# Optimization experiments

Measured on AMD Instinct MI355X. Metric: run time of the kernel, lower is better.

## Reference

```python
import jax, jax.numpy as jnp
import numpy as np

B, T, D = 2, 2048, 1024
H = 16
HD = D // H
NE = 17  # n_edge_types + 1

def setup_inputs() -> dict:
    key = jax.random.key(0)
    ks = jax.random.split(key, 6)
    x = jax.random.normal(ks[0], (B, T, D), dtype=jnp.float32)
    graph_adj = jax.random.uniform(ks[1], (B, T, T), dtype=jnp.float32)
    edge_types = jax.random.randint(ks[2], (B, T, T), 0, NE, dtype=jnp.int32)
    Wqkv = jax.random.normal(ks[3], (D, 3 * D), dtype=jnp.float32) * (D ** -0.5)
    Wproj = jax.random.normal(ks[4], (D, D), dtype=jnp.float32) * (D ** -0.5)
    adj_bias = jnp.zeros((H,), dtype=jnp.float32)
    edge_table = jax.random.normal(ks[5], (NE, H), dtype=jnp.float32) * 0.02
    return {"x": x, "graph_adj": graph_adj, "edge_types": edge_types,
            "Wqkv": Wqkv, "Wproj": Wproj, "adj_bias": adj_bias,
            "edge_table": edge_table}

def reference(x, graph_adj, edge_types, Wqkv, Wproj, adj_bias, edge_table):
    Bc, Tc, C = x.shape
    qkv = (x @ Wqkv).reshape(Bc, Tc, 3, H, HD)
    q, k, v = qkv[:, :, 0], qkv[:, :, 1], qkv[:, :, 2]  # [B,T,H,HD]
    scale = 1.0 / jnp.sqrt(jnp.asarray(HD, dtype=x.dtype))
    # scores: [B,H,T,T]
    attn = jnp.einsum('bqhd,bkhd->bhqk', q, k) * scale
    # adjacency bias per head
    attn = attn + adj_bias[None, :, None, None] * graph_adj[:, None, :, :]
    # edge-type bias: lookup [B,T,T,H] -> [B,H,T,T]
    etype_b = edge_table[edge_types]  # [B,T,T,H]
    attn = attn + jnp.transpose(etype_b, (0, 3, 1, 2))
    # causal mask (upper triangle, diag=1)
    causal = jnp.triu(jnp.ones((Tc, Tc), dtype=bool), k=1)
    attn = jnp.where(causal[None, None, :, :], jnp.asarray(-jnp.inf, dtype=attn.dtype), attn)
    attn = jax.nn.softmax(attn, axis=-1)
    out = jnp.einsum('bhqk,bkhd->bqhd', attn, v).reshape(Bc, Tc, C)
    return out @ Wproj
```

## Files before the change

kernel.cpp:

```cpp
#include <hip/hip_runtime.h>
#include <stdint.h>

#define TT 2048
#define HH 16
#define LOG2E 1.44269504089f

typedef _Float16 f16;
typedef __attribute__((ext_vector_type(8))) _Float16 f16x8;
typedef __attribute__((ext_vector_type(4))) float f32x4;
typedef unsigned short ushort_t;

__device__ __forceinline__ void gl_lds16(const void* g, void* l){
  __builtin_amdgcn_global_load_lds(
      (__attribute__((address_space(1))) void*)(void*)g,
      (__attribute__((address_space(3))) void*)l, 16, 0, 0);
}

__device__ __forceinline__ void lds_barrier(){
  __asm__ volatile("s_waitcnt lgkmcnt(0)\n\ts_barrier" ::: "memory");
}

template<int CTRL>
__device__ __forceinline__ float dpp_mov(float x){
  int xi = __builtin_bit_cast(int, x);
  return __builtin_bit_cast(float,
      __builtin_amdgcn_update_dpp(xi, xi, CTRL, 0xF, 0xF, false));
}
__device__ __forceinline__ float row_red_max(float x){
  x = fmaxf(x, dpp_mov<0xB1>(x));
  x = fmaxf(x, dpp_mov<0x4E>(x));
  x = fmaxf(x, dpp_mov<0x124>(x));
  x = fmaxf(x, dpp_mov<0x128>(x));
  return x;
}
__device__ __forceinline__ float row_red_sum(float x){
  x += dpp_mov<0xB1>(x);
  x += dpp_mov<0x4E>(x);
  x += dpp_mov<0x124>(x);
  x += dpp_mov<0x128>(x);
  return x;
}

struct SchedT { unsigned short v[80]; };
static constexpr SchedT make_sched(){
  SchedT s{};
  int idx = 0;
  for (int size = 8; size >= 1; --size){
    for (int qt = 31; qt >= 8; --qt){
      int full = qt >> 3;
      int tail = (qt & 7) + 1;
      if (size == 8)
        for (int ci = 0; ci < full; ++ci)
          s.v[idx++] = (unsigned short)(qt | (ci << 8));
      if (tail == size)
        s.v[idx++] = (unsigned short)(qt | (full << 8));
    }
    s.v[idx++] = (unsigned short)(size - 1);
  }
  return s;
}
__constant__ SchedT SCHED = make_sched();

__device__ __forceinline__ int slot_base(int qt){
  return (qt < 16) ? 2 * (qt - 8)
       : (qt < 24) ? 16 + 3 * (qt - 16)
                   : 40 + 4 * (qt - 24);
}

__global__ __launch_bounds__(256) void cvt_f2h_kernel(const float4* __restrict__ in,
                                                      uint2* __restrict__ out, int n4){
  int i = blockIdx.x * 256 + threadIdx.x;
  if (i >= n4) return;
  float4 v = in[i];
  union { f16 h[4]; uint2 u; } o;
  o.h[0] = (f16)v.x; o.h[1] = (f16)v.y; o.h[2] = (f16)v.z; o.h[3] = (f16)v.w;
  out[i] = o.u;
}

__global__ __launch_bounds__(256) void pack_bias_kernel(const float* __restrict__ gadj,
                                                        const int* __restrict__ etype,
                                                        uint32_t* __restrict__ out){
  int bid = blockIdx.x;
  int b = bid / 528, ti = bid - b * 528;
  int qt = (int)((sqrtf(8.f * (float)ti + 1.f) - 1.f) * 0.5f);
  while ((qt + 1) * (qt + 2) / 2 <= ti) ++qt;
  while (qt * (qt + 1) / 2 > ti) --qt;
  int kt = ti - qt * (qt + 1) / 2;

  int t = threadIdx.x;
  int row = t >> 2, c0 = (t & 3) << 4;
  size_t src = ((size_t)b * TT + qt * 64 + row) * TT + kt * 64 + c0;
  uint32_t* dst = out + (size_t)bid * 4096;
  int wq = (row >> 4) * 64 + ((row & 15) >> 2) * 16;
  int jbase = (t & 3) * 4 + (row & 3);
  #pragma unroll
  for (int v4 = 0; v4 < 4; ++v4){
    float4 g = *(const float4*)(gadj + src + v4 * 4);
    int4   e = *(const int4*)(etype + src + v4 * 4);
    union { f16 h; ushort_t u; } c;
    c.h = (f16)g.x; dst[(wq + v4 * 4 + 0) * 16 + jbase] = (uint32_t)c.u | ((uint32_t)e.x << 16);
    c.h = (f16)g.y; dst[(wq + v4 * 4 + 1) * 16 + jbase] = (uint32_t)c.u | ((uint32_t)e.y << 16);
    c.h = (f16)g.z; dst[(wq + v4 * 4 + 2) * 16 + jbase] = (uint32_t)c.u | ((uint32_t)e.z << 16);
    c.h = (f16)g.w; dst[(wq + v4 * 4 + 3) * 16 + jbase] = (uint32_t)c.u | ((uint32_t)e.w << 16);
  }
}

__global__ __launch_bounds__(256) void transpose_cvt_kernel(const float* __restrict__ in,
                                                            f16* __restrict__ out, int R, int C){
  __shared__ float tile[64][65];
  int c0 = blockIdx.x * 64, r0 = blockIdx.y * 64;
  int t = threadIdx.x;
  int row = t >> 2, cs = (t & 3) << 4;
  const float4* src = (const float4*)(in + (size_t)(r0 + row) * C + c0 + cs);
  float4 a = src[0], b = src[1], c = src[2], d = src[3];
  float* tr = &tile[row][cs];
  tr[0]=a.x; tr[1]=a.y; tr[2]=a.z;  tr[3]=a.w;
  tr[4]=b.x; tr[5]=b.y; tr[6]=b.z;  tr[7]=b.w;
  tr[8]=c.x; tr[9]=c.y; tr[10]=c.z; tr[11]=c.w;
  tr[12]=d.x;tr[13]=d.y;tr[14]=d.z; tr[15]=d.w;
  __syncthreads();
  f16 tmp[16];
  #pragma unroll
  for (int j = 0; j < 16; ++j) tmp[j] = (f16)tile[cs + j][row];
  f16* dst = out + (size_t)(c0 + row) * R + r0 + cs;
  *(uint4*)dst = *(uint4*)&tmp[0];
  *(uint4*)(dst + 8) = *(uint4*)&tmp[8];
}

template<int BN>
__global__ __launch_bounds__(256) void gemm_f16_kernel(const f16* __restrict__ A,
                                                       const f16* __restrict__ Bt,
                                                       void* __restrict__ Cout,
                                                       int M, int N, int K, int out_f32){
  constexpr int WN = BN / 2;
  constexpr int NI = WN / 16;
  __shared__ __align__(16) f16 As[128 * 32];
  __shared__ __align__(16) f16 Bs[BN * 32];
  int t = threadIdx.x;
  int w = t >> 6, lane = t & 63;
  int wm = (w >> 1) * 64, wn = (w & 1) * WN;
  int lrow = lane & 15, quad = lane >> 4;
  int bm = blockIdx.y, bn = blockIdx.x;

  f32x4 acc[4][NI];
  for (int i = 0; i < 4; ++i)
    for (int j = 0; j < NI; ++j)
      for (int r = 0; r < 4; ++r) acc[i][j][r] = 0.f;

  const int nk = K >> 5;
  for (int kt = 0; kt < nk; ++kt){
    int k0 = kt << 5;
    __syncthreads();
    #pragma unroll
    for (int i = 0; i < 2; ++i){
      int c = (w << 7) + (i << 6) + lane;
      gl_lds16(A + (size_t)((bm << 7) + (c >> 2)) * K + k0 + ((c & 3) << 3),
               As + ((w << 7) + (i << 6)) * 8);
      if constexpr (BN == 128){
        gl_lds16(Bt + (size_t)((bn << 7) + (c >> 2)) * K + k0 + ((c & 3) << 3),
                 Bs + ((w << 7) + (i << 6)) * 8);
      }
    }
    if constexpr (BN == 64){
      int c = (w << 6) + lane;
      gl_lds16(Bt + (size_t)((bn << 6) + (c >> 2)) * K + k0 + ((c & 3) << 3),
               Bs + (w << 6) * 8);
    }
    __syncthreads();
    f16x8 af[4], bfr[NI];
    #pragma unroll
    for (int mi = 0; mi < 4; ++mi)
      af[mi] = *(const f16x8*)(As + (wm + mi * 16 + lrow) * 32 + quad * 8);
    #pragma unroll
    for (int ni = 0; ni < NI; ++ni)
      bfr[ni] = *(const f16x8*)(Bs + (wn + ni * 16 + lrow) * 32 + quad * 8);
    #pragma unroll
    for (int mi = 0; mi < 4; ++mi)
      #pragma unroll
      for (int ni = 0; ni < NI; ++ni)
        acc[mi][ni] = __builtin_amdgcn_mfma_f32_16x16x32_f16(af[mi], bfr[ni], acc[mi][ni], 0, 0, 0);
  }

  #pragma unroll
  for (int mi = 0; mi < 4; ++mi)
    #pragma unroll
    for (int ni = 0; ni < NI; ++ni)
      #pragma unroll
      for (int r = 0; r < 4; ++r){
        int row = (bm << 7) + wm + mi * 16 + quad * 4 + r;
        int col = bn * BN + wn + ni * 16 + lrow;
        float val = acc[mi][ni][r];
        if (out_f32) ((float*)Cout)[(size_t)row * N + col] = val;
        else         ((f16*)Cout)[(size_t)row * N + col] = (f16)val;
      }
}

__global__ __launch_bounds__(256, 4) void attn_kernel(const f16* __restrict__ qkv,
                                                      const uint32_t* __restrict__ pbias,
                                                      const float* __restrict__ adj_bias,
                                                      const float* __restrict__ edge_table,
                                                      f16* __restrict__ attn_out,
                                                      f16* __restrict__ Opart,
                                                      float* __restrict__ MLpart){
  __shared__ __align__(16) f16 Ks[64 * 72];
  __shared__ __align__(16) f16 Vt[64 * 72];
  __shared__ __align__(16) f16 Ps[4][16 * 72];
  __shared__ float edge_lds[32 * 17];

  int bx = blockIdx.x;
  int bh = bx & 31;
  int h = bh & 15, b = bh >> 4;
  int ej = SCHED.v[bx >> 5];
  int qt = ej & 31, ci = ej >> 8;
  int ksrt = ci << 3;
  int kend = min(qt, ksrt + 7);
  bool whole = (qt < 8);

  int t = threadIdx.x;
  int w = t >> 6, lane = t & 63;
  int lrow = lane & 15, quad = lane >> 4;

  for (int i = t; i < 544; i += 256)
    edge_lds[i] = edge_table[(i % 17) * HH + h] * LOG2E;
  float adjb = adj_bias[h] * LOG2E;
  int erep = (lane & 31) * 17;

  int q0 = qt * 64 + w * 16;
  const size_t qrow = ((size_t)b * TT + q0 + lrow) * 3072 + h * 64;
  f16x8 qf0 = *(const f16x8*)(qkv + qrow + quad * 8);
  f16x8 qf1 = *(const f16x8*)(qkv + qrow + 32 + quad * 8);

  f32x4 o[4];
  for (int i = 0; i < 4; ++i)
    for (int r = 0; r < 4; ++r) o[i][r] = 0.f;
  float mrun[4] = {-1e30f, -1e30f, -1e30f, -1e30f};
  float lrun[4] = {0.f, 0.f, 0.f, 0.f};

  const int keyA = (t >> 3) << 1;
  const int hdA  = (t & 7) << 3;
  const int sA   = ((keyA >> 3) ^ (hdA >> 3)) & 7;
  const f16* kbase = qkv + (size_t)b * TT * 3072 + 1024 + h * 64;
  const f16* vbase = qkv + (size_t)b * TT * 3072 + 2048 + h * 64;
  const size_t koffA = (size_t)keyA * 3072 + hdA;
  const size_t koffB = koffA + 3072;

  const float SCL = 0.125f * LOG2E;

  const int tribase = b * 528 + ((qt * (qt + 1)) >> 1);
  const uint32_t* bthread = pbias + ((size_t)t << 4);
  const int qgb = q0 + quad * 4;

  uint4 ka, kb, va, vb;
  {
    const f16* kr = kbase + (size_t)(ksrt * 64) * 3072;
    const f16* vr = vbase + (size_t)(ksrt * 64) * 3072;
    ka = *(const uint4*)(kr + koffA); kb = *(const uint4*)(kr + koffB);
    va = *(const uint4*)(vr + koffA); vb = *(const uint4*)(vr + koffB);
  }

  for (int kt2 = ksrt; kt2 <= kend; ++kt2){
    lds_barrier();
    union B4 { uint4 v; uint32_t e[4]; } bb0, bb1, bb2, bb3;
    {
      const uint32_t* tp = bthread + ((size_t)(tribase + kt2) << 12);
      bb0.v = *(const uint4*)(tp + 0);
      bb1.v = *(const uint4*)(tp + 4);
      bb2.v = *(const uint4*)(tp + 8);
      bb3.v = *(const uint4*)(tp + 12);
    }
    *(uint4*)(Ks + keyA * 72 + hdA) = ka;
    *(uint4*)(Ks + (keyA + 1) * 72 + hdA) = kb;
    {
      union { uint4 u; f16 hh[8]; } ua, ub;
      ua.u = va; ub.u = vb;
      #pragma unroll
      for (int jj = 0; jj < 8; ++jj){
        union { f16 h[2]; uint32_t wv; } pr;
        pr.h[0] = ua.hh[jj]; pr.h[1] = ub.hh[jj];
        *(uint32_t*)(Vt + (hdA + jj) * 72 + (sA << 3) + (keyA & 7)) = pr.wv;
      }
    }
    if (kt2 < kend){
      const f16* kr = kbase + (size_t)((kt2 + 1) * 64) * 3072;
      const f16* vr = vbase + (size_t)((kt2 + 1) * 64) * 3072;
      ka = *(const uint4*)(kr + koffA); kb = *(const uint4*)(kr + koffB);
      va = *(const uint4*)(vr + koffA); vb = *(const uint4*)(vr + koffB);
    }
    lds_barrier();

    f32x4 sf[4];
    #pragma unroll
    for (int nb = 0; nb < 4; ++nb){
      f32x4 s = {0.f, 0.f, 0.f, 0.f};
      f16x8 kf0 = *(const f16x8*)(Ks + (nb * 16 + lrow) * 72 + quad * 8);
      f16x8 kf1 = *(const f16x8*)(Ks + (nb * 16 + lrow) * 72 + 32 + quad * 8);
      s = __builtin_amdgcn_mfma_f32_16x16x32_f16(qf0, kf0, s, 0, 0, 0);
      s = __builtin_amdgcn_mfma_f32_16x16x32_f16(qf1, kf1, s, 0, 0, 0);
      sf[nb] = s;
    }

    int kgb = kt2 * 64 + lrow;
    float sarr[4][4];
    bool diag = (kt2 == qt);
#define MASK_NB(nb, BB)                                                          \
    {                                                                            \
      int kg = kgb + nb * 16;                                                    \
      _Pragma("unroll")                                                          \
      for (int r = 0; r < 4; ++r){                                               \
        float v;                                                                 \
        if (diag && kg > qgb + r) v = -1e30f;                                    \
        else {                                                                   \
          uint32_t bp = BB.e[r];                                                 \
          union { ushort_t u; f16 h; } cv; cv.u = (ushort_t)bp;                  \
          v = sf[nb][r] * SCL + adjb * (float)cv.h + edge_lds[erep + (bp >> 16)];\
        }                                                                        \
        sarr[nb][r] = v;                                                         \
      }                                                                          \
    }
    MASK_NB(0, bb0)
    MASK_NB(1, bb1)
    MASK_NB(2, bb2)
    MASK_NB(3, bb3)
#undef MASK_NB

    float mx[4];
    bool need = false;
    #pragma unroll
    for (int r = 0; r < 4; ++r){
      float m_ = fmaxf(fmaxf(sarr[0][r], sarr[1][r]), fmaxf(sarr[2][r], sarr[3][r]));
      m_ = row_red_max(m_);
      mx[r] = m_;
      need = need || (m_ > mrun[r] + 5.0f);
    }
    if (__any(need)){
      #pragma unroll
      for (int r = 0; r < 4; ++r){
        float mnew = fmaxf(mrun[r], mx[r]);
        float alpha = exp2f(mrun[r] - mnew);
        lrun[r] *= alpha;
        #pragma unroll
        for (int nbh = 0; nbh < 4; ++nbh) o[nbh][r] *= alpha;
        mrun[r] = mnew;
      }
    }
    float pv_[4][4];
    #pragma unroll
    for (int r = 0; r < 4; ++r){
      float rs = 0.f;
      #pragma unroll
      for (int nb = 0; nb < 4; ++nb){
        float p = exp2f(sarr[nb][r] - mrun[r]);
        pv_[nb][r] = p; rs += p;
      }
      rs = row_red_sum(rs);
      lrun[r] += rs;
    }

    f16* Pw = &Ps[w][0];
    #pragma unroll
    for (int nb = 0; nb < 4; ++nb)
      #pragma unroll
      for (int r = 0; r < 4; ++r)
        Pw[(quad * 4 + r) * 72 + nb * 16 + lrow] = (f16)pv_[nb][r];
    __asm__ volatile("s_waitcnt lgkmcnt(0)" ::: "memory");

    #pragma unroll
    for (int cc = 0; cc < 2; ++cc){
      f16x8 pf = *(const f16x8*)(Pw + lrow * 72 + cc * 32 + quad * 8);
      #pragma unroll
      for (int nbh = 0; nbh < 4; ++nbh){
        int hd = nbh * 16 + lrow;
        int sb = (hd >> 3) & 7;
        f16x8 vf = *(const f16x8*)(Vt + hd * 72 + (((cc * 4 + quad) ^ sb) << 3));
        o[nbh] = __builtin_amdgcn_mfma_f32_16x16x32_f16(pf, vf, o[nbh], 0, 0, 0);
      }
    }
  }

  if (whole){
    float inv[4];
    #pragma unroll
    for (int r = 0; r < 4; ++r) inv[r] = 1.0f / lrun[r];
    #pragma unroll
    for (int nbh = 0; nbh < 4; ++nbh)
      #pragma unroll
      for (int r = 0; r < 4; ++r){
        int qg = q0 + quad * 4 + r;
        int col = h * 64 + nbh * 16 + lrow;
        attn_out[((size_t)b * TT + qg) * 1024 + col] = (f16)(o[nbh][r] * inv[r]);
      }
  } else {
    int slot = bh * 72 + slot_base(qt) + ci;
    f16* Ob = Opart + (size_t)slot * 4096;
    #pragma unroll
    for (int nbh = 0; nbh < 4; ++nbh)
      #pragma unroll
      for (int r = 0; r < 4; ++r)
        Ob[(w * 16 + quad * 4 + r) * 64 + nbh * 16 + lrow] = (f16)o[nbh][r];
    if (lrow == 0){
      #pragma unroll
      for (int r = 0; r < 4; ++r){
        int qq = w * 16 + quad * 4 + r;
        MLpart[(size_t)slot * 128 + qq] = mrun[r];
        MLpart[(size_t)slot * 128 + 64 + qq] = lrun[r];
      }
    }
  }
}

__global__ __launch_bounds__(256) void combine_kernel(const f16* __restrict__ Opart,
                                                      const float* __restrict__ ML,
                                                      f16* __restrict__ attn_out){
  int qt = blockIdx.x + 8;
  int bh = blockIdx.y;
  int nch = (qt >> 3) + 1;
  int slot0 = bh * 72 + slot_base(qt);
  int t = threadIdx.x;
  int q = t >> 2;
  int hd0 = (t & 3) << 4;

  float m[4], l[4];
  float M = -1e30f;
  #pragma unroll
  for (int c = 0; c < 4; ++c){
    if (c < nch){
      m[c] = ML[(size_t)(slot0 + c) * 128 + q];
      l[c] = ML[(size_t)(slot0 + c) * 128 + 64 + q];
      M = fmaxf(M, m[c]);
    } else { m[c] = -1e30f; l[c] = 0.f; }
  }
  float acc[16];
  #pragma unroll
  for (int i = 0; i < 16; ++i) acc[i] = 0.f;
  float L = 0.f;
  #pragma unroll
  for (int c = 0; c < 4; ++c){
    if (c < nch){
      float wgt = exp2f(m[c] - M);
      L += l[c] * wgt;
      const f16* O = Opart + (size_t)(slot0 + c) * 4096 + q * 64 + hd0;
      f16x8 a0 = *(const f16x8*)O, a1 = *(const f16x8*)(O + 8);
      #pragma unroll
      for (int i = 0; i < 8; ++i){
        acc[i]     += (float)a0[i] * wgt;
        acc[i + 8] += (float)a1[i] * wgt;
      }
    }
  }
  float invL = 1.0f / L;
  f16 outv[16];
  #pragma unroll
  for (int i = 0; i < 16; ++i) outv[i] = (f16)(acc[i] * invL);
  int b = bh >> 4, h = bh & 15;
  f16* dst = attn_out + ((size_t)b * TT + qt * 64 + q) * 1024 + h * 64 + hd0;
  *(uint4*)dst = *(uint4*)&outv[0];
  *(uint4*)(dst + 8) = *(uint4*)&outv[8];
}

extern "C" void kernel_launch(void* const* d_in, const int* in_sizes, int n_in,
                              void* d_out, int out_size, void* d_ws, size_t ws_size,
                              hipStream_t stream){
  (void)in_sizes; (void)n_in; (void)out_size; (void)ws_size;
  const float* x_f32  = (const float*)d_in[0];
  const float* gadj   = (const float*)d_in[1];
  const int*   etype  = (const int*)d_in[2];
  const float* wqkv   = (const float*)d_in[3];
  const float* wproj  = (const float*)d_in[4];
  const float* adjb   = (const float*)d_in[5];
  const float* etab   = (const float*)d_in[6];

  char* ws = (char*)d_ws;
  f16*     x_f16  = (f16*)(ws);
  f16*     qkv    = (f16*)(ws + (8u  << 20));
  f16*     wqkvT  = (f16*)(ws + (32u << 20));
  f16*     Opart  = (f16*)(ws + (32u << 20));
  f16*     wprojT = (f16*)(ws + (51u << 20));
  float*   MLpart = (float*)(ws + (53u << 20));
  uint32_t* pbias = (uint32_t*)(ws + (55u << 20));
  f16*     attn_o = x_f16;

  cvt_f2h_kernel<<<4096, 256, 0, stream>>>((const float4*)x_f32, (uint2*)x_f16, 1048576);
  pack_bias_kernel<<<1056, 256, 0, stream>>>(gadj, etype, pbias);
  transpose_cvt_kernel<<<dim3(48, 16), 256, 0, stream>>>(wqkv, wqkvT, 1024, 3072);
  transpose_cvt_kernel<<<dim3(16, 16), 256, 0, stream>>>(wproj, wprojT, 1024, 1024);
  gemm_f16_kernel<128><<<dim3(24, 32), 256, 0, stream>>>(x_f16, wqkvT, qkv, 4096, 3072, 1024, 0);
  attn_kernel<<<2560, 256, 0, stream>>>(qkv, pbias, adjb, etab, attn_o, Opart, MLpart);
  combine_kernel<<<dim3(24, 32), 256, 0, stream>>>(Opart, MLpart, attn_o);
  gemm_f16_kernel<64><<<dim3(16, 32), 256, 0, stream>>>(attn_o, wprojT, d_out, 4096, 1024, 1024, 1);
}
```

Before: 277.9 us.

## Compute transposed scores so P stays in registers for PV MFMA

Swaps the MFMA operand order so each lane holds scores for one query row across keys. Softmax statistics become one scalar per lane, reduced with two cross-lane shuffles instead of DPP row reductions. P is fed to a 16x16x16 MFMA directly from registers, which removes the LDS round trip and the Ps buffer. The bias-packing kernel is relaid out to match and now writes 16-byte vectors. In exchange the PV step uses twice as many smaller MFMAs with 8-byte V reads, and the rescale step needs per-row shuffles.

```diff
diff --git a/kernel.cpp b/kernel.cpp
--- a/kernel.cpp
+++ b/kernel.cpp
@@ -7,6 +7,7 @@
 
 typedef _Float16 f16;
 typedef __attribute__((ext_vector_type(8))) _Float16 f16x8;
+typedef __attribute__((ext_vector_type(4))) _Float16 f16x4;
 typedef __attribute__((ext_vector_type(4))) float f32x4;
 typedef unsigned short ushort_t;
 
@@ -18,27 +19,6 @@
 
 __device__ __forceinline__ void lds_barrier(){
   __asm__ volatile("s_waitcnt lgkmcnt(0)\n\ts_barrier" ::: "memory");
-}
-
-template<int CTRL>
-__device__ __forceinline__ float dpp_mov(float x){
-  int xi = __builtin_bit_cast(int, x);
-  return __builtin_bit_cast(float,
-      __builtin_amdgcn_update_dpp(xi, xi, CTRL, 0xF, 0xF, false));
-}
-__device__ __forceinline__ float row_red_max(float x){
-  x = fmaxf(x, dpp_mov<0xB1>(x));
-  x = fmaxf(x, dpp_mov<0x4E>(x));
-  x = fmaxf(x, dpp_mov<0x124>(x));
-  x = fmaxf(x, dpp_mov<0x128>(x));
-  return x;
-}
-__device__ __forceinline__ float row_red_sum(float x){
-  x += dpp_mov<0xB1>(x);
-  x += dpp_mov<0x4E>(x);
-  x += dpp_mov<0x124>(x);
-  x += dpp_mov<0x128>(x);
-  return x;
 }
 
 struct SchedT { unsigned short v[80]; };
@@ -91,17 +71,18 @@
   int row = t >> 2, c0 = (t & 3) << 4;
   size_t src = ((size_t)b * TT + qt * 64 + row) * TT + kt * 64 + c0;
   uint32_t* dst = out + (size_t)bid * 4096;
-  int wq = (row >> 4) * 64 + ((row & 15) >> 2) * 16;
-  int jbase = (t & 3) * 4 + (row & 3);
+  int wq = (row >> 4) * 64 + (row & 15);
   #pragma unroll
   for (int v4 = 0; v4 < 4; ++v4){
     float4 g = *(const float4*)(gadj + src + v4 * 4);
     int4   e = *(const int4*)(etype + src + v4 * 4);
     union { f16 h; ushort_t u; } c;
-    c.h = (f16)g.x; dst[(wq + v4 * 4 + 0) * 16 + jbase] = (uint32_t)c.u | ((uint32_t)e.x << 16);
-    c.h = (f16)g.y; dst[(wq + v4 * 4 + 1) * 16 + jbase] = (uint32_t)c.u | ((uint32_t)e.y << 16);
-    c.h = (f16)g.z; dst[(wq + v4 * 4 + 2) * 16 + jbase] = (uint32_t)c.u | ((uint32_t)e.z << 16);
-    c.h = (f16)g.w; dst[(wq + v4 * 4 + 3) * 16 + jbase] = (uint32_t)c.u | ((uint32_t)e.w << 16);
+    uint4 o;
+    c.h = (f16)g.x; o.x = (uint32_t)c.u | ((uint32_t)e.x << 16);
+    c.h = (f16)g.y; o.y = (uint32_t)c.u | ((uint32_t)e.y << 16);
+    c.h = (f16)g.z; o.z = (uint32_t)c.u | ((uint32_t)e.z << 16);
+    c.h = (f16)g.w; o.w = (uint32_t)c.u | ((uint32_t)e.w << 16);
+    *(uint4*)(dst + (((size_t)(wq + v4 * 16)) << 4) + ((t & 3) << 2)) = o;
   }
 }
 
@@ -204,7 +185,6 @@
                                                       float* __restrict__ MLpart){
   __shared__ __align__(16) f16 Ks[64 * 72];
   __shared__ __align__(16) f16 Vt[64 * 72];
-  __shared__ __align__(16) f16 Ps[4][16 * 72];
   __shared__ float edge_lds[32 * 17];
 
   int bx = blockIdx.x;
@@ -233,8 +213,7 @@
   f32x4 o[4];
   for (int i = 0; i < 4; ++i)
     for (int r = 0; r < 4; ++r) o[i][r] = 0.f;
-  float mrun[4] = {-1e30f, -1e30f, -1e30f, -1e30f};
-  float lrun[4] = {0.f, 0.f, 0.f, 0.f};
+  float mrun = -1e30f, lrun = 0.f;
 
   const int keyA = (t >> 3) << 1;
   const int hdA  = (t & 7) << 3;
@@ -248,7 +227,7 @@
 
   const int tribase = b * 528 + ((qt * (qt + 1)) >> 1);
   const uint32_t* bthread = pbias + ((size_t)t << 4);
-  const int qgb = q0 + quad * 4;
+  const int qg = q0 + lrow;
 
   uint4 ka, kb, va, vb;
   {
@@ -294,21 +273,20 @@
       f32x4 s = {0.f, 0.f, 0.f, 0.f};
       f16x8 kf0 = *(const f16x8*)(Ks + (nb * 16 + lrow) * 72 + quad * 8);
       f16x8 kf1 = *(const f16x8*)(Ks + (nb * 16 + lrow) * 72 + 32 + quad * 8);
-      s = __builtin_amdgcn_mfma_f32_16x16x32_f16(qf0, kf0, s, 0, 0, 0);
-      s = __builtin_amdgcn_mfma_f32_16x16x32_f16(qf1, kf1, s, 0, 0, 0);
+      s = __builtin_amdgcn_mfma_f32_16x16x32_f16(kf0, qf0, s, 0, 0, 0);
+      s = __builtin_amdgcn_mfma_f32_16x16x32_f16(kf1, qf1, s, 0, 0, 0);
       sf[nb] = s;
     }
 
-    int kgb = kt2 * 64 + lrow;
+    int kq = kt2 * 64 + quad * 4;
     float sarr[4][4];
     bool diag = (kt2 == qt);
 #define MASK_NB(nb, BB)                                                          \
     {                                                                            \
-      int kg = kgb + nb * 16;                                                    \
       _Pragma("unroll")                                                          \
       for (int r = 0; r < 4; ++r){                                               \
         float v;                                                                 \
-        if (diag && kg > qgb + r) v = -1e30f;                                    \
+        if (diag && (kq + nb * 16 + r > qg)) v = -1e30f;                         \
         else {                                                                   \
           uint32_t bp = BB.e[r];                                                 \
           union { ushort_t u; f16 h; } cv; cv.u = (ushort_t)bp;                  \
@@ -323,72 +301,71 @@
     MASK_NB(3, bb3)
 #undef MASK_NB
 
-    float mx[4];
-    bool need = false;
-    #pragma unroll
-    for (int r = 0; r < 4; ++r){
-      float m_ = fmaxf(fmaxf(sarr[0][r], sarr[1][r]), fmaxf(sarr[2][r], sarr[3][r]));
-      m_ = row_red_max(m_);
-      mx[r] = m_;
-      need = need || (m_ > mrun[r] + 5.0f);
-    }
+    float m_ = -1e30f;
+    #pragma unroll
+    for (int nb = 0; nb < 4; ++nb)
+      #pragma unroll
+      for (int r = 0; r < 4; ++r)
+        m_ = fmaxf(m_, sarr[nb][r]);
+    m_ = fmaxf(m_, __shfl_xor(m_, 16));
+    m_ = fmaxf(m_, __shfl_xor(m_, 32));
+    bool need = (m_ > mrun + 5.0f);
     if (__any(need)){
+      float mnew = fmaxf(mrun, m_);
+      float alpha = exp2f(mrun - mnew);
+      lrun *= alpha;
       #pragma unroll
       for (int r = 0; r < 4; ++r){
-        float mnew = fmaxf(mrun[r], mx[r]);
-        float alpha = exp2f(mrun[r] - mnew);
-        lrun[r] *= alpha;
+        float ar = __shfl(alpha, (quad << 2) | r);
         #pragma unroll
-        for (int nbh = 0; nbh < 4; ++nbh) o[nbh][r] *= alpha;
-        mrun[r] = mnew;
-      }
-    }
-    float pv_[4][4];
-    #pragma unroll
-    for (int r = 0; r < 4; ++r){
-      float rs = 0.f;
-      #pragma unroll
-      for (int nb = 0; nb < 4; ++nb){
-        float p = exp2f(sarr[nb][r] - mrun[r]);
-        pv_[nb][r] = p; rs += p;
-      }
-      rs = row_red_sum(rs);
-      lrun[r] += rs;
-    }
-
-    f16* Pw = &Ps[w][0];
+        for (int nbh = 0; nbh < 4; ++nbh) o[nbh][r] *= ar;
+      }
+      mrun = mnew;
+    }
+    float rs = 0.f;
     #pragma unroll
     for (int nb = 0; nb < 4; ++nb)
       #pragma unroll
-      for (int r = 0; r < 4; ++r)
-        Pw[(quad * 4 + r) * 72 + nb * 16 + lrow] = (f16)pv_[nb][r];
-    __asm__ volatile("s_waitcnt lgkmcnt(0)" ::: "memory");
-
-    #pragma unroll
-    for (int cc = 0; cc < 2; ++cc){
-      f16x8 pf = *(const f16x8*)(Pw + lrow * 72 + cc * 32 + quad * 8);
+      for (int r = 0; r < 4; ++r){
+        float p = exp2f(sarr[nb][r] - mrun);
+        sarr[nb][r] = p; rs += p;
+      }
+    rs += __shfl_xor(rs, 16);
+    rs += __shfl_xor(rs, 32);
+    lrun += rs;
+
+    f16x4 pa[4];
+    #pragma unroll
+    for (int nb = 0; nb < 4; ++nb){
+      pa[nb][0] = (f16)sarr[nb][0];
+      pa[nb][1] = (f16)sarr[nb][1];
+      pa[nb][2] = (f16)sarr[nb][2];
+      pa[nb][3] = (f16)sarr[nb][3];
+    }
+
+    #pragma unroll
+    for (int nb = 0; nb < 4; ++nb){
       #pragma unroll
       for (int nbh = 0; nbh < 4; ++nbh){
         int hd = nbh * 16 + lrow;
-        int sb = (hd >> 3) & 7;
-        f16x8 vf = *(const f16x8*)(Vt + hd * 72 + (((cc * 4 + quad) ^ sb) << 3));
-        o[nbh] = __builtin_amdgcn_mfma_f32_16x16x32_f16(pf, vf, o[nbh], 0, 0, 0);
+        int s2 = ((nb * 2 + (quad >> 1)) ^ (hd >> 3)) & 7;
+        f16x4 vf = *(const f16x4*)(Vt + hd * 72 + (s2 << 3) + ((quad & 1) << 2));
+        o[nbh] = __builtin_amdgcn_mfma_f32_16x16x16f16(pa[nb], vf, o[nbh], 0, 0, 0);
       }
     }
   }
 
   if (whole){
-    float inv[4];
-    #pragma unroll
-    for (int r = 0; r < 4; ++r) inv[r] = 1.0f / lrun[r];
-    #pragma unroll
-    for (int nbh = 0; nbh < 4; ++nbh)
-      #pragma unroll
-      for (int r = 0; r < 4; ++r){
-        int qg = q0 + quad * 4 + r;
+    #pragma unroll
+    for (int r = 0; r < 4; ++r){
+      float inv = 1.0f / __shfl(lrun, (quad << 2) | r);
+      int qg2 = q0 + quad * 4 + r;
+      #pragma unroll
+      for (int nbh = 0; nbh < 4; ++nbh){
         int col = h * 64 + nbh * 16 + lrow;
-        attn_out[((size_t)b * TT + qg) * 1024 + col] = (f16)(o[nbh][r] * inv[r]);
-      }
+        attn_out[((size_t)b * TT + qg2) * 1024 + col] = (f16)(o[nbh][r] * inv);
+      }
+    }
   } else {
     int slot = bh * 72 + slot_base(qt) + ci;
     f16* Ob = Opart + (size_t)slot * 4096;
@@ -397,13 +374,9 @@
       #pragma unroll
       for (int r = 0; r < 4; ++r)
         Ob[(w * 16 + quad * 4 + r) * 64 + nbh * 16 + lrow] = (f16)o[nbh][r];
-    if (lrow == 0){
-      #pragma unroll
-      for (int r = 0; r < 4; ++r){
-        int qq = w * 16 + quad * 4 + r;
-        MLpart[(size_t)slot * 128 + qq] = mrun[r];
-        MLpart[(size_t)slot * 128 + 64 + qq] = lrun[r];
-      }
+    if (quad == 0){
+      MLpart[(size_t)slot * 128 + w * 16 + lrow] = mrun;
+      MLpart[(size_t)slot * 128 + 64 + w * 16 + lrow] = lrun;
     }
   }
 }
```

Measured after the change: 281.9 us. No clear change (+1.4%).
